# Optimization experiments

Hardware: AMD Instinct MI355X
Metric: run time of the kernel (lower is better)

The kernel has to match this reference:

```python
import jax, jax.numpy as jnp
import numpy as np

# ---- multi-res 4D hash encoding config (Instant-NGP style) ----
L = 16                     # num_levels
T = 2 ** 19                # hash table entries per level (log2_hashmap_size)
FDIM = 2                   # features per entry (input_ch = L*2)
MIN_RES = np.array([16, 16, 16, 16], dtype=np.float64)
MAX_RES = np.array([256, 256, 256, 128], dtype=np.float64)
_growth = (MAX_RES / MIN_RES) ** (1.0 / (L - 1))
RES = np.floor(MIN_RES[None, :] * _growth[None, :] ** np.arange(L)[:, None]).astype(np.int32)  # [L,4]
PRIMES = np.array([1, 2654435761, 805459861, 3674653429], dtype=np.uint32)
# 16 corner offsets of the 4D hypercube
OFFS = np.array([[(c >> d) & 1 for d in range(4)] for c in range(16)], dtype=np.int32)  # [16,4]


def hash_encode(x, table):
    """x: [N,4] in [0,1); table: [L,T,FDIM] -> [N, L*FDIM]."""
    offs = jnp.asarray(OFFS)
    primes = jnp.asarray(PRIMES)
    outs = []
    for l in range(L):  # fixed small loop over levels
        res = jnp.asarray(RES[l], dtype=x.dtype)          # [4]
        pos = x * (res - 1.0)                              # [N,4]
        base = jnp.floor(pos)
        frac = pos - base                                  # [N,4]
        base_i = base.astype(jnp.int32)
        coord = jnp.clip(base_i[:, None, :] + offs[None], 0, jnp.asarray(RES[l] - 1))  # [N,16,4]
        h = coord.astype(jnp.uint32) * primes              # [N,16,4] u32 wraparound mult
        idx = (h[..., 0] ^ h[..., 1] ^ h[..., 2] ^ h[..., 3]) & jnp.uint32(T - 1)      # [N,16]
        feats = table[l][idx.astype(jnp.int32)]            # irregular gather -> [N,16,FDIM]
        # quadrilinear weights: prod over dims of frac / (1-frac)
        w = jnp.prod(jnp.where(offs[None] == 1, frac[:, None, :], 1.0 - frac[:, None, :]), axis=-1)  # [N,16]
        outs.append(jnp.einsum('nc,ncf->nf', w, feats))    # [N,FDIM]
    return jnp.concatenate(outs, axis=-1)                  # [N, L*FDIM]


def setup_inputs() -> dict:
    key = jax.random.key(0)
    ks = jax.random.split(key, 8)
    N = 1048576
    H = 64
    in_ch = L * FDIM  # 32
    x = jax.random.uniform(ks[0], (N, 4), dtype=jnp.float32)
    # NGP hash tables initialized uniform in [-1e-4, 1e-4]
    table = jax.random.uniform(ks[1], (L, T, FDIM), dtype=jnp.float32, minval=-1e-4, maxval=1e-4)
    def lin(k, out_d, in_d):
        b = 1.0 / np.sqrt(in_d)
        return jax.random.uniform(k, (out_d, in_d), dtype=jnp.float32, minval=-b, maxval=b)
    w0 = lin(ks[2], H, in_ch)
    w1 = lin(ks[3], H, H)
    w2 = lin(ks[4], H, H)
    w_out = lin(ks[5], 3, H)
    b_out = jax.random.uniform(ks[6], (3,), dtype=jnp.float32, minval=-1.0/np.sqrt(H), maxval=1.0/np.sqrt(H))
    return {"x": x, "table": table, "w0": w0, "w1": w1, "w2": w2, "w_out": w_out, "b_out": b_out}


def reference(x, table, w0, w1, w2, w_out, b_out):
    h = hash_encode(x, table)                 # [N, 32]
    for W in (w0, w1, w2):                    # bias-free Linear + ReLU x3
        h = jax.nn.relu(h @ W.T)
    v = h @ w_out.T + b_out                   # [N, 3]
    return v
```

## Files before the change

### kernel.cpp

```cpp
#include <hip/hip_runtime.h>
#include <math.h>

#define NLVL  16
#define TSZ   (1u << 19)
#define TMASK (TSZ - 1u)

struct ResArr { int m1[NLVL * 4]; };

typedef short  short8  __attribute__((ext_vector_type(8)));
typedef float  float4v __attribute__((ext_vector_type(4)));

static __device__ __forceinline__ unsigned short f2bf(float f) {
    unsigned u = __float_as_uint(f);
    return (unsigned short)((u + 0x7fffu + ((u >> 16) & 1u)) >> 16);
}

__global__ __launch_bounds__(256)
void cvt_table(const float4* __restrict__ t, uint2* __restrict__ o, int totalPairs)
{
    for (int i = blockIdx.x * 256 + (int)threadIdx.x; i < totalPairs;
         i += gridDim.x * 256) {
        const float4 e = t[i];
        o[i] = make_uint2((unsigned)f2bf(e.x) | ((unsigned)f2bf(e.y) << 16),
                          (unsigned)f2bf(e.z) | ((unsigned)f2bf(e.w) << 16));
    }
}

static __device__ __forceinline__
void encode_point_bf16(const float4*   __restrict__ x,
                       const unsigned* __restrict__ tbl,
                       unsigned*       __restrict__ featbf,
                       int N, int l, int n, const ResArr& res)
{
    if (n >= N) return;

    const float4 xv = x[n];
    const float px[4] = {xv.x, xv.y, xv.z, xv.w};

    int   bi[4];
    float fr[4], om[4];
    #pragma unroll
    for (int d = 0; d < 4; ++d) {
        const int r = res.m1[l * 4 + d];
        const float pos = px[d] * (float)r;
        const float fb  = floorf(pos);
        fr[d] = pos - fb;
        om[d] = 1.0f - fr[d];
        bi[d] = (int)fb;
    }
    const unsigned* tl  = tbl + (size_t)l * TSZ;
    const uint2*    tl2 = (const uint2*)tl;
    const uint4*    tl4 = (const uint4*)tl;

    unsigned hrest[8];
    #pragma unroll
    for (int p = 0; p < 8; ++p) {
        const int c1 = bi[1] + ( p       & 1);
        const int c2 = bi[2] + ((p >> 1) & 1);
        const int c3 = bi[3] + ((p >> 2) & 1);
        hrest[p] = ((unsigned)c1 * 2654435761u)
                 ^ ((unsigned)c2 * 805459861u)
                 ^ ((unsigned)c3 * 3674653429u);
    }

    const int b0 = bi[0];
    unsigned ea[8], eb[8];

    if ((b0 & 1) == 0) {
        #pragma unroll
        for (int p = 0; p < 8; ++p) {
            const unsigned h = ((unsigned)b0 ^ hrest[p]) & TMASK;
            const uint2 q = tl2[h >> 1];
            ea[p] = (h & 1u) ? q.y : q.x;
            eb[p] = (h & 1u) ? q.x : q.y;
        }
    } else if ((b0 & 3) == 1) {
        #pragma unroll
        for (int p = 0; p < 8; ++p) {
            const unsigned hA = ((unsigned)b0 ^ hrest[p]) & TMASK;
            const uint4 q = tl4[hA >> 2];
            const unsigned jA  = hA & 3u;
            const unsigned loA = (jA & 2u) ? q.z : q.x;
            const unsigned hiA = (jA & 2u) ? q.w : q.y;
            const unsigned loB = (jA & 2u) ? q.x : q.z;
            const unsigned hiB = (jA & 2u) ? q.y : q.w;
            ea[p] = (jA & 1u) ? hiA : loA;
            eb[p] = (jA & 1u) ? loB : hiB;
        }
    } else {
        #pragma unroll
        for (int p = 0; p < 8; ++p) {
            const unsigned hA = ((unsigned)b0       ^ hrest[p]) & TMASK;
            const unsigned hB = ((unsigned)(b0 + 1) ^ hrest[p]) & TMASK;
            ea[p] = tl[hA];
            eb[p] = tl[hB];
        }
    }

    float2 fv[16];
    #pragma unroll
    for (int p = 0; p < 8; ++p) {
        fv[2 * p]     = make_float2(__uint_as_float(ea[p] << 16),
                                    __uint_as_float(ea[p] & 0xffff0000u));
        fv[2 * p + 1] = make_float2(__uint_as_float(eb[p] << 16),
                                    __uint_as_float(eb[p] & 0xffff0000u));
    }

    float wt[16];
    #pragma unroll
    for (int c = 0; c < 16; ++c) {
        float w = ( c       & 1) ? fr[0] : om[0];
        w      *= ((c >> 1) & 1) ? fr[1] : om[1];
        w      *= ((c >> 2) & 1) ? fr[2] : om[2];
        w      *= ((c >> 3) & 1) ? fr[3] : om[3];
        wt[c] = w;
    }

    float a0 = 0.0f, a1 = 0.0f;
    #pragma unroll
    for (int c = 0; c < 16; ++c) {
        a0 = fmaf(wt[c], fv[c].x, a0);
        a1 = fmaf(wt[c], fv[c].y, a1);
    }
    featbf[(size_t)l * N + n] = (unsigned)f2bf(a0) | ((unsigned)f2bf(a1) << 16);
}

__global__ __launch_bounds__(256, 4)
void ingp_encode_bf16(const float4*   __restrict__ x,
                      const unsigned* __restrict__ tbl,
                      unsigned*       __restrict__ featbf,
                      int N, int chunksPerLevel, ResArr res)
{
    const int l     = blockIdx.x / chunksPerLevel;
    const int chunk = blockIdx.x - l * chunksPerLevel;
    encode_point_bf16(x, tbl, featbf, N, l, chunk * 256 + (int)threadIdx.x, res);
}

static __device__ __forceinline__
void encode_point_f32(const float4* __restrict__ x,
                      const float2* __restrict__ table,
                      unsigned*     __restrict__ featbf,
                      int N, int l, int n, const ResArr& res)
{
    if (n >= N) return;

    const float4 xv = x[n];
    const float px[4] = {xv.x, xv.y, xv.z, xv.w};

    int   bi[4];
    float fr[4], om[4];
    #pragma unroll
    for (int d = 0; d < 4; ++d) {
        const int r = res.m1[l * 4 + d];
        const float pos = px[d] * (float)r;
        const float fb  = floorf(pos);
        fr[d] = pos - fb;
        om[d] = 1.0f - fr[d];
        bi[d] = (int)fb;
    }
    const float2* tl  = table + (size_t)l * TSZ;
    const float4* tl4 = (const float4*)tl;

    unsigned hrest[8];
    #pragma unroll
    for (int p = 0; p < 8; ++p) {
        const int c1 = bi[1] + ( p       & 1);
        const int c2 = bi[2] + ((p >> 1) & 1);
        const int c3 = bi[3] + ((p >> 2) & 1);
        hrest[p] = ((unsigned)c1 * 2654435761u)
                 ^ ((unsigned)c2 * 805459861u)
                 ^ ((unsigned)c3 * 3674653429u);
    }

    float2 fv[16];
    if ((bi[0] & 1) == 0) {
        #pragma unroll
        for (int p = 0; p < 8; ++p) {
            const unsigned h = ((unsigned)bi[0] ^ hrest[p]) & TMASK;
            const float4 q = tl4[h >> 1];
            const bool odd = (h & 1);
            fv[2 * p]     = odd ? make_float2(q.z, q.w) : make_float2(q.x, q.y);
            fv[2 * p + 1] = odd ? make_float2(q.x, q.y) : make_float2(q.z, q.w);
        }
    } else {
        #pragma unroll
        for (int p = 0; p < 8; ++p) {
            const unsigned hA = ((unsigned)bi[0]       ^ hrest[p]) & TMASK;
            const unsigned hB = ((unsigned)(bi[0] + 1) ^ hrest[p]) & TMASK;
            fv[2 * p]     = tl[hA];
            fv[2 * p + 1] = tl[hB];
        }
    }

    float wt[16];
    #pragma unroll
    for (int c = 0; c < 16; ++c) {
        float w = ( c       & 1) ? fr[0] : om[0];
        w      *= ((c >> 1) & 1) ? fr[1] : om[1];
        w      *= ((c >> 2) & 1) ? fr[2] : om[2];
        w      *= ((c >> 3) & 1) ? fr[3] : om[3];
        wt[c] = w;
    }

    float a0 = 0.0f, a1 = 0.0f;
    #pragma unroll
    for (int c = 0; c < 16; ++c) {
        a0 = fmaf(wt[c], fv[c].x, a0);
        a1 = fmaf(wt[c], fv[c].y, a1);
    }
    featbf[(size_t)l * N + n] = (unsigned)f2bf(a0) | ((unsigned)f2bf(a1) << 16);
}

__global__ __launch_bounds__(256, 4)
void ingp_encode_f32(const float4* __restrict__ x,
                     const float2* __restrict__ table,
                     unsigned*     __restrict__ featbf,
                     int N, int chunksPerLevel, ResArr res)
{
    const int l     = blockIdx.x / chunksPerLevel;
    const int chunk = blockIdx.x - l * chunksPerLevel;
    encode_point_f32(x, table, featbf, N, l, chunk * 256 + (int)threadIdx.x, res);
}

#define TILE_BODY(P0, A0)                                                     \
{                                                                             \
    asm volatile("" : "+v"(idx0));    \
    float4v acc0[4];                                                          \
    _Pragma("unroll")                                                         \
    for (int t = 0; t < 4; ++t) {                                             \
        acc0[t] = (float4v){0.f, 0.f, 0.f, 0.f};                              \
        acc0[t] = __builtin_amdgcn_mfma_f32_16x16x32_bf16(A0, w0f[t], acc0[t], 0, 0, 0); \
    }                                                                         \
    _Pragma("unroll")                                                         \
    for (int t = 0; t < 4; ++t)                                               \
        _Pragma("unroll")                                                     \
        for (int r = 0; r < 4; ++r)                                           \
            *(unsigned short*)(hbase + (q * 4 + r) * 144 + (t * 16 + nn) * 2) = \
                f2bf(fmaxf(acc0[t][r], 0.0f));                                \
    short8 a1[2];                                                             \
    _Pragma("unroll")                                                         \
    for (int s = 0; s < 2; ++s)                                               \
        a1[s] = *(const short8*)(hbase + nn * 144 + s * 64 + q * 16);         \
    float4v acc1[4];                                                          \
    _Pragma("unroll")                                                         \
    for (int t = 0; t < 4; ++t) {                                             \
        acc1[t] = (float4v){0.f, 0.f, 0.f, 0.f};                              \
        _Pragma("unroll")                                                     \
        for (int s = 0; s < 2; ++s)                                           \
            acc1[t] = __builtin_amdgcn_mfma_f32_16x16x32_bf16(a1[s], w1f[s][t], acc1[t], 0, 0, 0); \
    }                                                                         \
    _Pragma("unroll")                                                         \
    for (int t = 0; t < 4; ++t)                                               \
        _Pragma("unroll")                                                     \
        for (int r = 0; r < 4; ++r)                                           \
            *(unsigned short*)(hbase + (q * 4 + r) * 144 + (t * 16 + nn) * 2) = \
                f2bf(fmaxf(acc1[t][r], 0.0f));                                \
    short8 a2[2];                                                             \
    _Pragma("unroll")                                                         \
    for (int s = 0; s < 2; ++s)                                               \
        a2[s] = *(const short8*)(hbase + nn * 144 + s * 64 + q * 16);         \
    float4v acc2[4];                                                          \
    _Pragma("unroll")                                                         \
    for (int t = 0; t < 4; ++t) {                                             \
        acc2[t] = (float4v){0.f, 0.f, 0.f, 0.f};                              \
        _Pragma("unroll")                                                     \
        for (int s = 0; s < 2; ++s) {                                         \
            const short8 w2x = *(const short8*)(wlds + ((s * 4 + t) * 64 + lane) * 16 + idx0); \
            acc2[t] = __builtin_amdgcn_mfma_f32_16x16x32_bf16(a2[s], w2x, acc2[t], 0, 0, 0); \
        }                                                                     \
    }                                                                         \
    _Pragma("unroll")                                                         \
    for (int t = 0; t < 4; ++t)                                               \
        _Pragma("unroll")                                                     \
        for (int r = 0; r < 4; ++r)                                           \
            *(unsigned short*)(hbase + (q * 4 + r) * 144 + (t * 16 + nn) * 2) = \
                f2bf(fmaxf(acc2[t][r], 0.0f));                                \
    short8 a3[2];                                                             \
    _Pragma("unroll")                                                         \
    for (int s = 0; s < 2; ++s)                                               \
        a3[s] = *(const short8*)(hbase + nn * 144 + s * 64 + q * 16);         \
    float4v oc = (float4v){0.f, 0.f, 0.f, 0.f};                               \
    _Pragma("unroll")                                                         \
    for (int s = 0; s < 2; ++s) {                                             \
        const short8 wox = *(const short8*)(wlds + ((8 + s) * 64 + lane) * 16 + idx0); \
        oc = __builtin_amdgcn_mfma_f32_16x16x32_bf16(a3[s], wox, oc, 0, 0, 0); \
    }                                                                         \
    if (nn < 3) {                                                             \
        _Pragma("unroll")                                                     \
        for (int r = 0; r < 4; ++r) {                                         \
            const int pt = (P0) + q * 4 + r;                                  \
            if (pt < N) out[pt * 3 + nn] = oc[r] + bias;                      \
        }                                                                     \
    }                                                                         \
}

__global__ __launch_bounds__(256, 4)
void ingp_mlp_mfma(const unsigned* __restrict__ featbf,
                   const float*    __restrict__ w0,
                   const float*    __restrict__ w1,
                   const float*    __restrict__ w2,
                   const float*    __restrict__ wout,
                   const float*    __restrict__ bout,
                   float*          __restrict__ out,
                   int N)
{
    __shared__ char lds_raw[4 * 16 * 144];
    __shared__ char wlds[(8 + 2) * 64 * 16];

    const int tid  = (int)threadIdx.x;
    const int wave = tid >> 6;
    const int lane = tid & 63;
    const int q    = lane >> 4;
    const int nn   = lane & 15;
    char* hbase = lds_raw + wave * (16 * 144);

    if (tid < 64) {
        #pragma unroll
        for (int s = 0; s < 2; ++s)
            #pragma unroll
            for (int t = 0; t < 4; ++t) {
                const float* wr2 = w2 + (t * 16 + nn) * 64 + s * 32 + q * 8;
                short8 f;
                #pragma unroll
                for (int e = 0; e < 8; ++e) f[e] = (short)f2bf(wr2[e]);
                *(short8*)(wlds + ((s * 4 + t) * 64 + lane) * 16) = f;
            }
        #pragma unroll
        for (int s = 0; s < 2; ++s) {
            short8 f;
            #pragma unroll
            for (int e = 0; e < 8; ++e)
                f[e] = (nn < 3) ? (short)f2bf(wout[nn * 64 + s * 32 + q * 8 + e])
                                : (short)0;
            *(short8*)(wlds + ((8 + s) * 64 + lane) * 16) = f;
        }
    }
    __syncthreads();

    short8 w0f[4];
    #pragma unroll
    for (int t = 0; t < 4; ++t) {
        const float* wr = w0 + (t * 16 + nn) * 32 + q * 8;
        #pragma unroll
        for (int e = 0; e < 8; ++e) w0f[t][e] = (short)f2bf(wr[e]);
    }
    short8 w1f[2][4];
    #pragma unroll
    for (int s = 0; s < 2; ++s)
        #pragma unroll
        for (int t = 0; t < 4; ++t) {
            const float* wr1 = w1 + (t * 16 + nn) * 64 + s * 32 + q * 8;
            #pragma unroll
            for (int e = 0; e < 8; ++e) w1f[s][t][e] = (short)f2bf(wr1[e]);
        }
    const float bias = (nn < 3) ? bout[nn] : 0.0f;

    int idx0 = 0;

    const int base = (int)blockIdx.x * 32 + wave * 8;

    unsigned ufA[4], ufB[4];
    {
        const int pA = (base * 16 < N) ? (base * 16 + nn) : 0;
        const int pB = ((base + 1) * 16 < N) ? ((base + 1) * 16 + nn) : 0;
        #pragma unroll
        for (int v = 0; v < 4; ++v) {
            ufA[v] = featbf[(size_t)(q * 4 + v) * N + pA];
            ufB[v] = featbf[(size_t)(q * 4 + v) * N + pB];
        }
    }

    for (int it = 0; it < 8; it += 2) {
        const int p0A = (base + it) * 16;
        if (p0A >= N) break;

        short8 a0A;
        #pragma unroll
        for (int v = 0; v < 4; ++v) {
            a0A[2 * v]     = (short)(ufA[v] & 0xffffu);
            a0A[2 * v + 1] = (short)(ufA[v] >> 16);
        }
        {
            const int p0n = (base + it + 2) * 16;
            const bool more = (it + 2 < 8) && (p0n < N);
            const int pn = more ? (p0n + nn) : 0;
            #pragma unroll
            for (int v = 0; v < 4; ++v)
                ufA[v] = featbf[(size_t)(q * 4 + v) * N + pn];
        }
        TILE_BODY(p0A, a0A)

        const int p0B = (base + it + 1) * 16;
        if (p0B < N) {
            short8 a0B;
            #pragma unroll
            for (int v = 0; v < 4; ++v) {
                a0B[2 * v]     = (short)(ufB[v] & 0xffffu);
                a0B[2 * v + 1] = (short)(ufB[v] >> 16);
            }
            {
                const int p0n = (base + it + 3) * 16;
                const bool more = (it + 3 < 8) && (p0n < N);
                const int pn = more ? (p0n + nn) : 0;
                #pragma unroll
                for (int v = 0; v < 4; ++v)
                    ufB[v] = featbf[(size_t)(q * 4 + v) * N + pn];
            }
            TILE_BODY(p0B, a0B)
        }
    }
}

__global__ __launch_bounds__(256, 2)
void ingp_fused(const float4* __restrict__ x,
                const float2* __restrict__ table,
                const float*  __restrict__ w0,
                const float*  __restrict__ w1,
                const float*  __restrict__ w2,
                const float*  __restrict__ wout,
                const float*  __restrict__ bout,
                float*        __restrict__ out,
                int N, ResArr res)
{
    const int n = blockIdx.x * blockDim.x + threadIdx.x;
    if (n >= N) return;

    const float4 xv = x[n];
    const float px[4] = {xv.x, xv.y, xv.z, xv.w};

    float h1[64];
    #pragma unroll
    for (int j = 0; j < 64; ++j) h1[j] = 0.0f;

    float a0p = 0.0f, a1p = 0.0f;

    #pragma unroll 1
    for (int l = 0; l < NLVL; ++l) {
        int   rm[4], bi[4];
        float fr[4], om[4];
        #pragma unroll
        for (int d = 0; d < 4; ++d) {
            const int r = res.m1[l * 4 + d];
            rm[d] = r;
            const float pos = px[d] * (float)r;
            const float fb  = floorf(pos);
            fr[d] = pos - fb;
            om[d] = 1.0f - fr[d];
            bi[d] = (int)fb;
        }
        const float2* tl = table + (size_t)l * TSZ;

        float2 fv[16];
        float  wt[16];
        #pragma unroll
        for (int c = 0; c < 16; ++c) {
            int c0 = bi[0] + ( c       & 1);
            int c1 = bi[1] + ((c >> 1) & 1);
            int c2 = bi[2] + ((c >> 2) & 1);
            int c3 = bi[3] + ((c >> 3) & 1);
            c0 = min(max(c0, 0), rm[0]);
            c1 = min(max(c1, 0), rm[1]);
            c2 = min(max(c2, 0), rm[2]);
            c3 = min(max(c3, 0), rm[3]);
            const unsigned hh = (unsigned)c0
                              ^ ((unsigned)c1 * 2654435761u)
                              ^ ((unsigned)c2 * 805459861u)
                              ^ ((unsigned)c3 * 3674653429u);
            fv[c] = tl[hh & TMASK];
            float w = ( c       & 1) ? fr[0] : om[0];
            w      *= ((c >> 1) & 1) ? fr[1] : om[1];
            w      *= ((c >> 2) & 1) ? fr[2] : om[2];
            w      *= ((c >> 3) & 1) ? fr[3] : om[3];
            wt[c] = w;
        }
        {
            const int lp = (l == 0) ? 0 : (l - 1);
            const float* w0c = w0 + 2 * lp;
            #pragma unroll
            for (int j = 0; j < 64; ++j)
                h1[j] = fmaf(w0c[j * 32], a0p, fmaf(w0c[j * 32 + 1], a1p, h1[j]));
        }
        float a0 = 0.0f, a1 = 0.0f;
        #pragma unroll
        for (int c = 0; c < 16; ++c) {
            a0 = fmaf(wt[c], fv[c].x, a0);
            a1 = fmaf(wt[c], fv[c].y, a1);
        }
        a0p = a0; a1p = a1;
    }
    {
        const float* w0c = w0 + 2 * (NLVL - 1);
        #pragma unroll
        for (int j = 0; j < 64; ++j)
            h1[j] = fmaf(w0c[j * 32], a0p, fmaf(w0c[j * 32 + 1], a1p, h1[j]));
    }
    #pragma unroll
    for (int j = 0; j < 64; ++j) h1[j] = fmaxf(h1[j], 0.0f);

    float h2[64];
    #pragma unroll
    for (int j = 0; j < 64; ++j) {
        float acc = 0.0f;
        const float* wr = w1 + j * 64;
        #pragma unroll
        for (int i = 0; i < 64; ++i) acc = fmaf(wr[i], h1[i], acc);
        h2[j] = fmaxf(acc, 0.0f);
    }
    float h3[64];
    #pragma unroll
    for (int j = 0; j < 64; ++j) {
        float acc = 0.0f;
        const float* wr = w2 + j * 64;
        #pragma unroll
        for (int i = 0; i < 64; ++i) acc = fmaf(wr[i], h2[i], acc);
        h3[j] = fmaxf(acc, 0.0f);
    }
    float o[3];
    #pragma unroll
    for (int k = 0; k < 3; ++k) {
        float acc = bout[k];
        const float* wr = wout + k * 64;
        #pragma unroll
        for (int i = 0; i < 64; ++i) acc = fmaf(wr[i], h3[i], acc);
        o[k] = acc;
    }
    out[n * 3 + 0] = o[0];
    out[n * 3 + 1] = o[1];
    out[n * 3 + 2] = o[2];
}

extern "C" void kernel_launch(void* const* d_in, const int* in_sizes, int n_in,
                              void* d_out, int out_size, void* d_ws, size_t ws_size,
                              hipStream_t stream) {
    (void)n_in; (void)out_size;

    const float* x     = (const float*)d_in[0];
    const float* table = (const float*)d_in[1];
    const float* w0    = (const float*)d_in[2];
    const float* w1    = (const float*)d_in[3];
    const float* w2    = (const float*)d_in[4];
    const float* wout  = (const float*)d_in[5];
    const float* bout  = (const float*)d_in[6];
    float* out = (float*)d_out;

    const int N = in_sizes[0] / 4;

    ResArr res;
    for (int d = 0; d < 4; ++d) {
        const double minr = 16.0;
        const double maxr = (d == 3) ? 128.0 : 256.0;
        const double growth = pow(maxr / minr, 1.0 / (double)(NLVL - 1));
        for (int l = 0; l < NLVL; ++l) {
            const int r = (int)floor(minr * pow(growth, (double)l));
            res.m1[l * 4 + d] = r - 1;
        }
    }

    const size_t tblBytes  = (size_t)NLVL * TSZ * sizeof(unsigned);
    const size_t featBytes = (size_t)NLVL * (size_t)N * sizeof(unsigned);
    const int chunksPerLevel = (N + 255) / 256;

    if (ws_size >= tblBytes + featBytes) {
        unsigned* tblbf  = (unsigned*)d_ws;
        unsigned* featbf = (unsigned*)((char*)d_ws + tblBytes);

        hipLaunchKernelGGL(cvt_table, dim3(2048), dim3(256), 0, stream,
                           (const float4*)table, (uint2*)tblbf,
                           (int)(NLVL * TSZ / 2));

        hipLaunchKernelGGL(ingp_encode_bf16, dim3(NLVL * chunksPerLevel), dim3(256),
                           0, stream, (const float4*)x, tblbf,
                           featbf, N, chunksPerLevel, res);

        const int tiles  = (N + 15) / 16;
        const int waves  = (tiles + 7) / 8;
        const int blocks = (waves + 3) / 4;
        hipLaunchKernelGGL(ingp_mlp_mfma, dim3(blocks), dim3(256), 0, stream,
                           featbf, w0, w1, w2, wout, bout, out, N);
    } else if (ws_size >= featBytes) {
        unsigned* featbf = (unsigned*)d_ws;
        hipLaunchKernelGGL(ingp_encode_f32, dim3(NLVL * chunksPerLevel), dim3(256),
                           0, stream, (const float4*)x, (const float2*)table,
                           featbf, N, chunksPerLevel, res);

        const int tiles  = (N + 15) / 16;
        const int waves  = (tiles + 7) / 8;
        const int blocks = (waves + 3) / 4;
        hipLaunchKernelGGL(ingp_mlp_mfma, dim3(blocks), dim3(256), 0, stream,
                           featbf, w0, w1, w2, wout, bout, out, N);
    } else {
        hipLaunchKernelGGL(ingp_fused, dim3((N + 255) / 256), dim3(256), 0, stream,
                           (const float4*)x, (const float2*)table,
                           w0, w1, w2, wout, bout, out, N, res);
    }
}
```

Before: 728.8 us.

## Interleave two MLP tiles per wave with separate LDS staging buffers

The MFMA MLP kernel used to run tile A's full layer chain and then tile B's. It now runs each layer on both tiles together, with a separate LDS scratch region per tile. The aim is to hide MFMA and LDS round-trip latency through independent instruction streams and to reuse each w2/wout fragment load across both tiles. In exchange it doubles LDS scratch and register use, and lowers the launch-bounds occupancy hint from 4 to 3 blocks.

```diff
diff --git a/kernel.cpp b/kernel.cpp
--- a/kernel.cpp
+++ b/kernel.cpp
@@ -222,79 +222,20 @@
     encode_point_f32(x, table, featbf, N, l, chunk * 256 + (int)threadIdx.x, res);
 }
 
-#define TILE_BODY(P0, A0)                                                     \
-{                                                                             \
-    asm volatile("" : "+v"(idx0));    \
-    float4v acc0[4];                                                          \
-    _Pragma("unroll")                                                         \
-    for (int t = 0; t < 4; ++t) {                                             \
-        acc0[t] = (float4v){0.f, 0.f, 0.f, 0.f};                              \
-        acc0[t] = __builtin_amdgcn_mfma_f32_16x16x32_bf16(A0, w0f[t], acc0[t], 0, 0, 0); \
-    }                                                                         \
+#define STORE_H(HB, AC)                                                       \
     _Pragma("unroll")                                                         \
     for (int t = 0; t < 4; ++t)                                               \
         _Pragma("unroll")                                                     \
         for (int r = 0; r < 4; ++r)                                           \
-            *(unsigned short*)(hbase + (q * 4 + r) * 144 + (t * 16 + nn) * 2) = \
-                f2bf(fmaxf(acc0[t][r], 0.0f));                                \
-    short8 a1[2];                                                             \
+            *(unsigned short*)((HB) + (q * 4 + r) * 144 + (t * 16 + nn) * 2) =\
+                f2bf(fmaxf((AC)[t][r], 0.0f));
+
+#define READ_A(HB, DST)                                                       \
     _Pragma("unroll")                                                         \
     for (int s = 0; s < 2; ++s)                                               \
-        a1[s] = *(const short8*)(hbase + nn * 144 + s * 64 + q * 16);         \
-    float4v acc1[4];                                                          \
-    _Pragma("unroll")                                                         \
-    for (int t = 0; t < 4; ++t) {                                             \
-        acc1[t] = (float4v){0.f, 0.f, 0.f, 0.f};                              \
-        _Pragma("unroll")                                                     \
-        for (int s = 0; s < 2; ++s)                                           \
-            acc1[t] = __builtin_amdgcn_mfma_f32_16x16x32_bf16(a1[s], w1f[s][t], acc1[t], 0, 0, 0); \
-    }                                                                         \
-    _Pragma("unroll")                                                         \
-    for (int t = 0; t < 4; ++t)                                               \
-        _Pragma("unroll")                                                     \
-        for (int r = 0; r < 4; ++r)                                           \
-            *(unsigned short*)(hbase + (q * 4 + r) * 144 + (t * 16 + nn) * 2) = \
-                f2bf(fmaxf(acc1[t][r], 0.0f));                                \
-    short8 a2[2];                                                             \
-    _Pragma("unroll")                                                         \
-    for (int s = 0; s < 2; ++s)                                               \
-        a2[s] = *(const short8*)(hbase + nn * 144 + s * 64 + q * 16);         \
-    float4v acc2[4];                                                          \
-    _Pragma("unroll")                                                         \
-    for (int t = 0; t < 4; ++t) {                                             \
-        acc2[t] = (float4v){0.f, 0.f, 0.f, 0.f};                              \
-        _Pragma("unroll")                                                     \
-        for (int s = 0; s < 2; ++s) {                                         \
-            const short8 w2x = *(const short8*)(wlds + ((s * 4 + t) * 64 + lane) * 16 + idx0); \
-            acc2[t] = __builtin_amdgcn_mfma_f32_16x16x32_bf16(a2[s], w2x, acc2[t], 0, 0, 0); \
-        }                                                                     \
-    }                                                                         \
-    _Pragma("unroll")                                                         \
-    for (int t = 0; t < 4; ++t)                                               \
-        _Pragma("unroll")                                                     \
-        for (int r = 0; r < 4; ++r)                                           \
-            *(unsigned short*)(hbase + (q * 4 + r) * 144 + (t * 16 + nn) * 2) = \
-                f2bf(fmaxf(acc2[t][r], 0.0f));                                \
-    short8 a3[2];                                                             \
-    _Pragma("unroll")                                                         \
-    for (int s = 0; s < 2; ++s)                                               \
-        a3[s] = *(const short8*)(hbase + nn * 144 + s * 64 + q * 16);         \
-    float4v oc = (float4v){0.f, 0.f, 0.f, 0.f};                               \
-    _Pragma("unroll")                                                         \
-    for (int s = 0; s < 2; ++s) {                                             \
-        const short8 wox = *(const short8*)(wlds + ((8 + s) * 64 + lane) * 16 + idx0); \
-        oc = __builtin_amdgcn_mfma_f32_16x16x32_bf16(a3[s], wox, oc, 0, 0, 0); \
-    }                                                                         \
-    if (nn < 3) {                                                             \
-        _Pragma("unroll")                                                     \
-        for (int r = 0; r < 4; ++r) {                                         \
-            const int pt = (P0) + q * 4 + r;                                  \
-            if (pt < N) out[pt * 3 + nn] = oc[r] + bias;                      \
-        }                                                                     \
-    }                                                                         \
-}
-
-__global__ __launch_bounds__(256, 4)
+        (DST)[s] = *(const short8*)((HB) + nn * 144 + s * 64 + q * 16);
+
+__global__ __launch_bounds__(256, 3)
 void ingp_mlp_mfma(const unsigned* __restrict__ featbf,
                    const float*    __restrict__ w0,
                    const float*    __restrict__ w1,
@@ -304,7 +245,7 @@
                    float*          __restrict__ out,
                    int N)
 {
-    __shared__ char lds_raw[4 * 16 * 144];
+    __shared__ char lds_raw[4 * 2 * 16 * 144];
     __shared__ char wlds[(8 + 2) * 64 * 16];
 
     const int tid  = (int)threadIdx.x;
@@ -312,7 +253,8 @@
     const int lane = tid & 63;
     const int q    = lane >> 4;
     const int nn   = lane & 15;
-    char* hbase = lds_raw + wave * (16 * 144);
+    char* hbA = lds_raw + wave * (2 * 16 * 144);
+    char* hbB = hbA + 16 * 144;
 
     if (tid < 64) {
         #pragma unroll
@@ -373,40 +315,116 @@
     for (int it = 0; it < 8; it += 2) {
         const int p0A = (base + it) * 16;
         if (p0A >= N) break;
-
-        short8 a0A;
+        const int p0B = (base + it + 1) * 16;
+        const bool hasB = (p0B < N);
+
+        short8 a0A, a0B;
         #pragma unroll
         for (int v = 0; v < 4; ++v) {
             a0A[2 * v]     = (short)(ufA[v] & 0xffffu);
             a0A[2 * v + 1] = (short)(ufA[v] >> 16);
+            a0B[2 * v]     = (short)(ufB[v] & 0xffffu);
+            a0B[2 * v + 1] = (short)(ufB[v] >> 16);
         }
         {
-            const int p0n = (base + it + 2) * 16;
-            const bool more = (it + 2 < 8) && (p0n < N);
-            const int pn = more ? (p0n + nn) : 0;
-            #pragma unroll
-            for (int v = 0; v < 4; ++v)
-                ufA[v] = featbf[(size_t)(q * 4 + v) * N + pn];
-        }
-        TILE_BODY(p0A, a0A)
-
-        const int p0B = (base + it + 1) * 16;
-        if (p0B < N) {
-            short8 a0B;
+            const int pA2 = (base + it + 2) * 16;
+            const int pB2 = (base + it + 3) * 16;
+            const bool mA = (it + 2 < 8) && (pA2 < N);
+            const bool mB = (it + 3 < 8) && (pB2 < N);
+            const int iA = mA ? (pA2 + nn) : 0;
+            const int iB = mB ? (pB2 + nn) : 0;
             #pragma unroll
             for (int v = 0; v < 4; ++v) {
-                a0B[2 * v]     = (short)(ufB[v] & 0xffffu);
-                a0B[2 * v + 1] = (short)(ufB[v] >> 16);
+                ufA[v] = featbf[(size_t)(q * 4 + v) * N + iA];
+                ufB[v] = featbf[(size_t)(q * 4 + v) * N + iB];
             }
-            {
-                const int p0n = (base + it + 3) * 16;
-                const bool more = (it + 3 < 8) && (p0n < N);
-                const int pn = more ? (p0n + nn) : 0;
+        }
+
+        asm volatile("" : "+v"(idx0));
+
+        float4v acA[4], acB[4];
+        #pragma unroll
+        for (int t = 0; t < 4; ++t) {
+            acA[t] = (float4v){0.f, 0.f, 0.f, 0.f};
+            acA[t] = __builtin_amdgcn_mfma_f32_16x16x32_bf16(a0A, w0f[t], acA[t], 0, 0, 0);
+        }
+        if (hasB) {
+            #pragma unroll
+            for (int t = 0; t < 4; ++t) {
+                acB[t] = (float4v){0.f, 0.f, 0.f, 0.f};
+                acB[t] = __builtin_amdgcn_mfma_f32_16x16x32_bf16(a0B, w0f[t], acB[t], 0, 0, 0);
+            }
+        }
+        STORE_H(hbA, acA)
+        if (hasB) { STORE_H(hbB, acB) }
+        short8 a1A[2], a1B[2];
+        READ_A(hbA, a1A)
+        if (hasB) { READ_A(hbB, a1B) }
+
+        #pragma unroll
+        for (int t = 0; t < 4; ++t) {
+            acA[t] = (float4v){0.f, 0.f, 0.f, 0.f};
+            #pragma unroll
+            for (int s = 0; s < 2; ++s)
+                acA[t] = __builtin_amdgcn_mfma_f32_16x16x32_bf16(a1A[s], w1f[s][t], acA[t], 0, 0, 0);
+        }
+        if (hasB) {
+            #pragma unroll
+            for (int t = 0; t < 4; ++t) {
+                acB[t] = (float4v){0.f, 0.f, 0.f, 0.f};
                 #pragma unroll
-                for (int v = 0; v < 4; ++v)
-                    ufB[v] = featbf[(size_t)(q * 4 + v) * N + pn];
+                for (int s = 0; s < 2; ++s)
+                    acB[t] = __builtin_amdgcn_mfma_f32_16x16x32_bf16(a1B[s], w1f[s][t], acB[t], 0, 0, 0);
             }
-            TILE_BODY(p0B, a0B)
+        }
+        STORE_H(hbA, acA)
+        if (hasB) { STORE_H(hbB, acB) }
+        short8 a2A[2], a2B[2];
+        READ_A(hbA, a2A)
+        if (hasB) { READ_A(hbB, a2B) }
+
+        #pragma unroll
+        for (int t = 0; t < 4; ++t) {
+            acA[t] = (float4v){0.f, 0.f, 0.f, 0.f};
+            acB[t] = (float4v){0.f, 0.f, 0.f, 0.f};
+        }
+        #pragma unroll
+        for (int s = 0; s < 2; ++s)
+            #pragma unroll
+            for (int t = 0; t < 4; ++t) {
+                const short8 w2x = *(const short8*)(wlds + ((s * 4 + t) * 64 + lane) * 16 + idx0);
+                acA[t] = __builtin_amdgcn_mfma_f32_16x16x32_bf16(a2A[s], w2x, acA[t], 0, 0, 0);
+                if (hasB)
+                    acB[t] = __builtin_amdgcn_mfma_f32_16x16x32_bf16(a2B[s], w2x, acB[t], 0, 0, 0);
+            }
+        STORE_H(hbA, acA)
+        if (hasB) { STORE_H(hbB, acB) }
+        short8 a3A[2], a3B[2];
+        READ_A(hbA, a3A)
+        if (hasB) { READ_A(hbB, a3B) }
+
+        float4v ocA = (float4v){0.f, 0.f, 0.f, 0.f};
+        float4v ocB = (float4v){0.f, 0.f, 0.f, 0.f};
+        #pragma unroll
+        for (int s = 0; s < 2; ++s) {
+            const short8 wox = *(const short8*)(wlds + ((8 + s) * 64 + lane) * 16 + idx0);
+            ocA = __builtin_amdgcn_mfma_f32_16x16x32_bf16(a3A[s], wox, ocA, 0, 0, 0);
+            if (hasB)
+                ocB = __builtin_amdgcn_mfma_f32_16x16x32_bf16(a3B[s], wox, ocB, 0, 0, 0);
+        }
+        if (nn < 3) {
+            #pragma unroll
+            for (int r = 0; r < 4; ++r) {
+                const int pt = p0A + q * 4 + r;
+                if (pt < N) out[pt * 3 + nn] = ocA[r] + bias;
+            }
+            if (hasB) {
+                #pragma unroll
+                for (int r = 0; r < 4; ++r) {
+                    const int pt = p0B + q * 4 + r;
+                    if (pt < N) out[pt * 3 + nn] = ocB[r] + bias;
+                }
+            }
         }
     }
 }
```

Result: no change. 728.8 us (-0.0%).
